# Optimization experiments

Measured on AMD Instinct MI355X. Metric: run time of the kernel, lower is better.

## Reference

```python
import jax, jax.numpy as jnp
import numpy as np

B, S, H = 4, 2048, 1024

def setup_inputs() -> dict:
    key = jax.random.key(0)
    ks = jax.random.split(key, 6)
    scale = 1.0 / np.sqrt(H)
    return {
        "query": jax.random.normal(ks[0], (B, S, H), dtype=jnp.float32),
        "key":   jax.random.normal(ks[1], (B, S, H), dtype=jnp.float32),
        "value": jax.random.normal(ks[2], (B, S, H), dtype=jnp.float32),
        "Wq": jax.random.normal(ks[3], (H, H), dtype=jnp.float32) * scale,
        "Wk": jax.random.normal(ks[4], (H, H), dtype=jnp.float32) * scale,
        "Wv": jax.random.normal(ks[5], (H, H), dtype=jnp.float32) * scale,
    }

def reference(query, key, value, Wq, Wk, Wv):
    # nn.Linear(bias=False): y = x @ W.T
    q = jnp.einsum('bsh,oh->bso', query, Wq)
    k = jnp.einsum('bsh,oh->bso', key, Wk)
    v = jnp.einsum('bsh,oh->bso', value, Wv)
    # full QK^T scores [B, Q, K], scaled by sqrt(hidden_size)
    scores = jnp.einsum('bqh,bkh->bqk', q, k) / jnp.sqrt(jnp.asarray(H, q.dtype))
    attn = jax.nn.softmax(scores, axis=2)
    return jnp.einsum('bqk,bkh->bqh', attn, v)
```

## Files before the change

### kernel.cpp

```cpp
#include <hip/hip_runtime.h>
#include <hip/hip_bf16.h>
#include <stdint.h>

#define BATCH 4
#define SLEN  2048
#define HID   1024

typedef __attribute__((ext_vector_type(8))) short bfrag8;
typedef __attribute__((ext_vector_type(4))) float facc4;

__device__ __forceinline__ unsigned short f2b(float f) {
  union { float f; unsigned int i; } x; x.f = f;
  unsigned int r = x.i + 0x7FFFu + ((x.i >> 16) & 1u);
  return (unsigned short)(r >> 16);
}
__device__ __forceinline__ unsigned int pk2(float a, float b) {
  unsigned int ua = __float_as_uint(a) + 0x8000u;
  unsigned int ub = __float_as_uint(b) + 0x8000u;
  return (ua >> 16) | (ub & 0xFFFF0000u);
}

__device__ __forceinline__ void gl_lds16(const void* g, void* l) {
  __builtin_amdgcn_global_load_lds(
      (const __attribute__((address_space(1))) void*)g,
      (__attribute__((address_space(3))) void*)l, 16, 0, 0);
}

__global__ __launch_bounds__(256) void qkv_proj(
    const float* __restrict__ q, const float* __restrict__ k,
    const float* __restrict__ v, const float* __restrict__ wq,
    const float* __restrict__ wk, const float* __restrict__ wv,
    unsigned short* __restrict__ Qb, unsigned short* __restrict__ Kb,
    unsigned short* __restrict__ Vt, float* __restrict__ lsum) {
  const int pid = blockIdx.x;
  if (pid < 8) {
    float4 z = {0.f, 0.f, 0.f, 0.f};
    ((float4*)lsum)[pid * 256 + threadIdx.x] = z;
  }
  const int p2     = (pid & 7) * 192 + (pid >> 3);
  const int g      = p2 >> 9;
  const int within = p2 & 511;

  const float* A; const float* B; unsigned short* C;
  long bm, bn; int ldc_;
  if (g == 0)      { A = q;  B = wq; C = Qb; }
  else if (g == 1) { A = k;  B = wk; C = Kb; }
  else             { A = wv; B = v;  C = Vt; }
  if (g < 2) {
    const int gid = within >> 5, rem = within & 31;
    bm = (long)(gid * 4 + (rem & 3)) * 128;
    bn = (long)(rem >> 2) * 128;
    ldc_ = 1024;
  } else {
    const int gid = within >> 8, rem = within & 255;
    bm = (long)(gid * 4 + (rem & 3)) * 128;
    bn = (long)(rem >> 2) * 128;
    ldc_ = 8192;
  }

  __shared__ __align__(16) unsigned short As[128 * 64];
  __shared__ __align__(16) unsigned short Bs[128 * 64];

  const int tid  = threadIdx.x;
  const int lane = tid & 63;
  const int wave = tid >> 6;
  const int wr   = (wave >> 1) * 64;
  const int wc   = (wave & 1) * 64;
  const int ln   = lane & 15;
  const int lq   = lane >> 4;
  const int swz  = ln & 7;

  facc4 acc[4][4] = {};

  const float* ap[4]; const float* bp[4];
  unsigned short* asd[4]; unsigned short* bsd[4];
#pragma unroll
  for (int j = 0; j < 4; ++j) {
    const int c   = j * 256 + tid;
    const int row = c >> 3;
    const int src = ((c & 7) ^ (row & 7)) * 8;
    ap[j]  = A + (bm + row) * 1024 + src;
    bp[j]  = B + (bn + row) * 1024 + src;
    asd[j] = &As[c * 8];
    bsd[j] = &Bs[c * 8];
  }

  for (int k0 = 0; k0 < 1024; k0 += 64) {
#pragma unroll
    for (int j = 0; j < 4; ++j) {
      const float4* a4 = (const float4*)ap[j];
      const float4* b4 = (const float4*)bp[j];
      float4 xa0 = a4[0], xa1 = a4[1];
      float4 xb0 = b4[0], xb1 = b4[1];
      ap[j] += 64; bp[j] += 64;
      uint4 wa = { pk2(xa0.x, xa0.y), pk2(xa0.z, xa0.w),
                   pk2(xa1.x, xa1.y), pk2(xa1.z, xa1.w) };
      uint4 wb = { pk2(xb0.x, xb0.y), pk2(xb0.z, xb0.w),
                   pk2(xb1.x, xb1.y), pk2(xb1.z, xb1.w) };
      *(uint4*)asd[j] = wa;
      *(uint4*)bsd[j] = wb;
    }
    __syncthreads();

#pragma unroll
    for (int kk = 0; kk < 2; ++kk) {
      bfrag8 af[4], bfr[4];
#pragma unroll
      for (int i = 0; i < 4; ++i)
        af[i] = *(const bfrag8*)&As[(wr + i * 16 + ln) * 64 + ((kk * 4 + lq) ^ swz) * 8];
#pragma unroll
      for (int j = 0; j < 4; ++j)
        bfr[j] = *(const bfrag8*)&Bs[(wc + j * 16 + ln) * 64 + ((kk * 4 + lq) ^ swz) * 8];
#pragma unroll
      for (int i = 0; i < 4; ++i)
#pragma unroll
        for (int j = 0; j < 4; ++j)
          acc[i][j] = __builtin_amdgcn_mfma_f32_16x16x32_bf16(af[i], bfr[j], acc[i][j], 0, 0, 0);
    }
    __syncthreads();
  }

#pragma unroll
  for (int i = 0; i < 4; ++i)
#pragma unroll
    for (int j = 0; j < 4; ++j) {
      const long m = bm + wr + i * 16 + lq * 4;
      const long n = bn + wc + j * 16 + ln;
#pragma unroll
      for (int r = 0; r < 4; ++r)
        C[(m + r) * (long)ldc_ + n] = f2b(acc[i][j][r]);
    }
}

template <int MODE, typename OutT>
__global__ __launch_bounds__(256) void gemm_nt(
    const unsigned short* __restrict__ A, const unsigned short* __restrict__ B,
    OutT* __restrict__ C, int K, int lda, int ldb, int ldc,
    long aStrideZ, long bStrideZ, long cStrideZ, float alpha,
    float* __restrict__ lsum) {
  A += (long)blockIdx.z * aStrideZ;
  B += (long)blockIdx.z * bStrideZ;
  C += (long)blockIdx.z * cStrideZ;
  const long lz = (long)blockIdx.z * SLEN;

  const int nbm = gridDim.x, nbn = gridDim.y;
  const int nb  = nbm * nbn;
  const int pid = blockIdx.y * nbm + blockIdx.x;
  const int p2  = (pid & 7) * (nb >> 3) + (pid >> 3);
  const int GROUP = 4;
  const int gsize = GROUP * nbn;
  const int gid   = p2 / gsize;
  const int rem   = p2 - gid * gsize;
  const long bm = (long)(gid * GROUP + (rem & (GROUP - 1))) * 128;
  const long bn = (long)(rem >> 2) * 128;

  __shared__ __align__(16) unsigned short As[128 * 64];
  __shared__ __align__(16) unsigned short Bs[128 * 64];

  const int tid  = threadIdx.x;
  const int lane = tid & 63;
  const int wave = tid >> 6;
  const int wr   = (wave >> 1) * 64;
  const int wc   = (wave & 1) * 64;
  const int ln   = lane & 15;
  const int lq   = lane >> 4;
  const int swz  = ln & 7;

  facc4 acc[4][4] = {};

  const unsigned short* ap[4]; const unsigned short* bp[4];
  unsigned short* asd[4]; unsigned short* bsd[4];
#pragma unroll
  for (int j = 0; j < 4; ++j) {
    const int c   = j * 256 + tid;
    const int row = c >> 3;
    const int src = ((c & 7) ^ (row & 7)) * 8;
    ap[j]  = A + (bm + row) * (long)lda + src;
    bp[j]  = B + (bn + row) * (long)ldb + src;
    asd[j] = &As[c * 8];
    bsd[j] = &Bs[c * 8];
  }

  for (int k0 = 0; k0 < K; k0 += 64) {
#pragma unroll
    for (int j = 0; j < 4; ++j) { gl_lds16(ap[j], asd[j]); ap[j] += 64; }
#pragma unroll
    for (int j = 0; j < 4; ++j) { gl_lds16(bp[j], bsd[j]); bp[j] += 64; }
    __syncthreads();

#pragma unroll
    for (int kk = 0; kk < 2; ++kk) {
      bfrag8 af[4], bfr[4];
#pragma unroll
      for (int i = 0; i < 4; ++i)
        af[i] = *(const bfrag8*)&As[(wr + i * 16 + ln) * 64 + ((kk * 4 + lq) ^ swz) * 8];
#pragma unroll
      for (int j = 0; j < 4; ++j)
        bfr[j] = *(const bfrag8*)&Bs[(wc + j * 16 + ln) * 64 + ((kk * 4 + lq) ^ swz) * 8];
#pragma unroll
      for (int i = 0; i < 4; ++i)
#pragma unroll
        for (int j = 0; j < 4; ++j)
          acc[i][j] = __builtin_amdgcn_mfma_f32_16x16x32_bf16(af[i], bfr[j], acc[i][j], 0, 0, 0);
    }
    __syncthreads();
  }

  if constexpr (MODE == 1) {
#pragma unroll
    for (int i = 0; i < 4; ++i) {
#pragma unroll
      for (int r = 0; r < 4; ++r) {
        const long m = bm + wr + i * 16 + lq * 4 + r;
        float rowsum = 0.f;
#pragma unroll
        for (int j = 0; j < 4; ++j) {
          const long n = bn + wc + j * 16 + ln;
          float e = __expf(acc[i][j][r] * alpha);
          C[m * (long)ldc + n] = (OutT)f2b(e);
          rowsum += e;
        }
        rowsum += __shfl_xor(rowsum, 1, 64);
        rowsum += __shfl_xor(rowsum, 2, 64);
        rowsum += __shfl_xor(rowsum, 4, 64);
        rowsum += __shfl_xor(rowsum, 8, 64);
        if (ln == 0) atomicAdd(&lsum[lz + m], rowsum);
      }
    }
  } else {
    float inv[16];
#pragma unroll
    for (int i = 0; i < 4; ++i)
#pragma unroll
      for (int r = 0; r < 4; ++r)
        inv[i * 4 + r] = 1.0f / lsum[lz + bm + wr + i * 16 + lq * 4 + r];
#pragma unroll
    for (int i = 0; i < 4; ++i)
#pragma unroll
      for (int j = 0; j < 4; ++j) {
        const long m = bm + wr + i * 16 + lq * 4;
        const long n = bn + wc + j * 16 + ln;
#pragma unroll
        for (int r = 0; r < 4; ++r)
          ((float*)C)[(m + r) * (long)ldc + n] = acc[i][j][r] * inv[i * 4 + r];
      }
  }
}

extern "C" void kernel_launch(void* const* d_in, const int* in_sizes, int n_in,
                              void* d_out, int out_size, void* d_ws, size_t ws_size,
                              hipStream_t stream) {
  const float* q_in = (const float*)d_in[0];
  const float* k_in = (const float*)d_in[1];
  const float* v_in = (const float*)d_in[2];
  const float* wq   = (const float*)d_in[3];
  const float* wk   = (const float*)d_in[4];
  const float* wv   = (const float*)d_in[5];
  float* out = (float*)d_out;

  const long NXH = (long)BATCH * SLEN * HID;
  const long SH  = (long)SLEN * HID;
  const long SS  = (long)SLEN * SLEN;

  unsigned short* ws  = (unsigned short*)d_ws;
  unsigned short* Qb  = ws;
  unsigned short* Kb  = Qb + NXH;
  unsigned short* Vt  = Kb + NXH;
  float*          lsum = (float*)(Vt + NXH);
  unsigned short* P   = (unsigned short*)(lsum + 8192);

  const dim3 blk(256);

  qkv_proj<<<dim3(1536), blk, 0, stream>>>(q_in, k_in, v_in, wq, wk, wv,
                                           Qb, Kb, Vt, lsum);

  gemm_nt<1, unsigned short><<<dim3(16, 16, BATCH), blk, 0, stream>>>(
      Qb, Kb, P, HID, HID, HID, SLEN, SH, SH, SS, 0.03125f, lsum);

  gemm_nt<2, float><<<dim3(16, 8, BATCH), blk, 0, stream>>>(
      P, Vt, out, SLEN, SLEN, BATCH * SLEN, HID, SS, SLEN, SH, 1.0f, lsum);
}
```

Before: 329.2 us.

## Pre-cast inputs and weights to bf16, then use direct global-to-LDS loads in projection

Adds a separate elementwise kernel that converts the fp32 activations and weights to bf16 in workspace. The projection GEMM then stages its tiles with global_load_lds DMA instead of loading fp32 into registers, converting and storing to LDS. This removes the redundant per-tile fp32 reads and conversions, since each input element was re-read by many tiles. The cost is an extra full read/write pass over roughly 27M floats and an extra launch. The P buffer now aliases the cast-input region, and rounding changes from round-half-up to round-to-nearest-even.

```diff
diff --git a/kernel.cpp b/kernel.cpp
--- a/kernel.cpp
+++ b/kernel.cpp
@@ -8,17 +8,13 @@
 
 typedef __attribute__((ext_vector_type(8))) short bfrag8;
 typedef __attribute__((ext_vector_type(4))) float facc4;
+typedef __attribute__((ext_vector_type(4))) unsigned short us4;
 
 __device__ __forceinline__ unsigned short f2b(float f) {
   union { float f; unsigned int i; } x; x.f = f;
   unsigned int r = x.i + 0x7FFFu + ((x.i >> 16) & 1u);
   return (unsigned short)(r >> 16);
 }
-__device__ __forceinline__ unsigned int pk2(float a, float b) {
-  unsigned int ua = __float_as_uint(a) + 0x8000u;
-  unsigned int ub = __float_as_uint(b) + 0x8000u;
-  return (ua >> 16) | (ub & 0xFFFF0000u);
-}
 
 __device__ __forceinline__ void gl_lds16(const void* g, void* l) {
   __builtin_amdgcn_global_load_lds(
@@ -26,26 +22,48 @@
       (__attribute__((address_space(3))) void*)l, 16, 0, 0);
 }
 
-__global__ __launch_bounds__(256) void qkv_proj(
+__global__ __launch_bounds__(256) void cast_all(
     const float* __restrict__ q, const float* __restrict__ k,
     const float* __restrict__ v, const float* __restrict__ wq,
     const float* __restrict__ wk, const float* __restrict__ wv,
+    us4* __restrict__ dst, float* __restrict__ lsum) {
+  if (blockIdx.x < 8) {
+    float4 z = {0.f, 0.f, 0.f, 0.f};
+    ((float4*)lsum)[blockIdx.x * 256 + threadIdx.x] = z;
+  }
+  const long i = (long)blockIdx.x * 256 + threadIdx.x;
+  const long S1 = 2097152, S2 = 4194304, S3 = 6291456,
+             S4 = 6553600, S5 = 6815744;
+  const float4* src; long off;
+  if (i < S2) {
+    if (i < S1) { src = (const float4*)q;  off = i; }
+    else        { src = (const float4*)k;  off = i - S1; }
+  } else if (i < S3) { src = (const float4*)v;  off = i - S2; }
+  else if   (i < S4) { src = (const float4*)wq; off = i - S3; }
+  else if   (i < S5) { src = (const float4*)wk; off = i - S4; }
+  else               { src = (const float4*)wv; off = i - S5; }
+  float4 x = src[off];
+  us4 o;
+  o.x = f2b(x.x); o.y = f2b(x.y); o.z = f2b(x.z); o.w = f2b(x.w);
+  dst[i] = o;
+}
+
+__global__ __launch_bounds__(256) void proj3(
+    const unsigned short* __restrict__ Xq, const unsigned short* __restrict__ Wqb,
+    const unsigned short* __restrict__ Xk, const unsigned short* __restrict__ Wkb,
+    const unsigned short* __restrict__ Xv, const unsigned short* __restrict__ Wvb,
     unsigned short* __restrict__ Qb, unsigned short* __restrict__ Kb,
-    unsigned short* __restrict__ Vt, float* __restrict__ lsum) {
+    unsigned short* __restrict__ Vt) {
   const int pid = blockIdx.x;
-  if (pid < 8) {
-    float4 z = {0.f, 0.f, 0.f, 0.f};
-    ((float4*)lsum)[pid * 256 + threadIdx.x] = z;
-  }
   const int p2     = (pid & 7) * 192 + (pid >> 3);
   const int g      = p2 >> 9;
   const int within = p2 & 511;
 
-  const float* A; const float* B; unsigned short* C;
+  const unsigned short* A; const unsigned short* B; unsigned short* C;
   long bm, bn; int ldc_;
-  if (g == 0)      { A = q;  B = wq; C = Qb; }
-  else if (g == 1) { A = k;  B = wk; C = Kb; }
-  else             { A = wv; B = v;  C = Vt; }
+  if (g == 0)      { A = Xq; B = Wqb; C = Qb; }
+  else if (g == 1) { A = Xk; B = Wkb; C = Kb; }
+  else             { A = Wvb; B = Xv; C = Vt; }
   if (g < 2) {
     const int gid = within >> 5, rem = within & 31;
     bm = (long)(gid * 4 + (rem & 3)) * 128;
@@ -72,7 +90,7 @@
 
   facc4 acc[4][4] = {};
 
-  const float* ap[4]; const float* bp[4];
+  const unsigned short* ap[4]; const unsigned short* bp[4];
   unsigned short* asd[4]; unsigned short* bsd[4];
 #pragma unroll
   for (int j = 0; j < 4; ++j) {
@@ -87,19 +105,9 @@
 
   for (int k0 = 0; k0 < 1024; k0 += 64) {
 #pragma unroll
-    for (int j = 0; j < 4; ++j) {
-      const float4* a4 = (const float4*)ap[j];
-      const float4* b4 = (const float4*)bp[j];
-      float4 xa0 = a4[0], xa1 = a4[1];
-      float4 xb0 = b4[0], xb1 = b4[1];
-      ap[j] += 64; bp[j] += 64;
-      uint4 wa = { pk2(xa0.x, xa0.y), pk2(xa0.z, xa0.w),
-                   pk2(xa1.x, xa1.y), pk2(xa1.z, xa1.w) };
-      uint4 wb = { pk2(xb0.x, xb0.y), pk2(xb0.z, xb0.w),
-                   pk2(xb1.x, xb1.y), pk2(xb1.z, xb1.w) };
-      *(uint4*)asd[j] = wa;
-      *(uint4*)bsd[j] = wb;
-    }
+    for (int j = 0; j < 4; ++j) { gl_lds16(ap[j], asd[j]); ap[j] += 64; }
+#pragma unroll
+    for (int j = 0; j < 4; ++j) { gl_lds16(bp[j], bsd[j]); bp[j] += 64; }
     __syncthreads();
 
 #pragma unroll
@@ -259,20 +267,29 @@
   float* out = (float*)d_out;
 
   const long NXH = (long)BATCH * SLEN * HID;
+  const long NW  = (long)HID * HID;
   const long SH  = (long)SLEN * HID;
   const long SS  = (long)SLEN * SLEN;
 
-  unsigned short* ws  = (unsigned short*)d_ws;
-  unsigned short* Qb  = ws;
-  unsigned short* Kb  = Qb + NXH;
-  unsigned short* Vt  = Kb + NXH;
+  unsigned short* ws = (unsigned short*)d_ws;
+  unsigned short* Xq  = ws;
+  unsigned short* Xk  = Xq  + NXH;
+  unsigned short* Xv  = Xk  + NXH;
+  unsigned short* Wqb = Xv  + NXH;
+  unsigned short* Wkb = Wqb + NW;
+  unsigned short* Wvb = Wkb + NW;
+  unsigned short* Qb  = Wvb + NW;
+  unsigned short* Kb  = Qb  + NXH;
+  unsigned short* Vt  = Kb  + NXH;
   float*          lsum = (float*)(Vt + NXH);
-  unsigned short* P   = (unsigned short*)(lsum + 8192);
+  unsigned short* P   = Xq;
 
   const dim3 blk(256);
 
-  qkv_proj<<<dim3(1536), blk, 0, stream>>>(q_in, k_in, v_in, wq, wk, wv,
-                                           Qb, Kb, Vt, lsum);
+  cast_all<<<dim3(27648), blk, 0, stream>>>(q_in, k_in, v_in, wq, wk, wv,
+                                            (us4*)ws, lsum);
+
+  proj3<<<dim3(1536), blk, 0, stream>>>(Xq, Wqb, Xk, Wkb, Xv, Wvb, Qb, Kb, Vt);
 
   gemm_nt<1, unsigned short><<<dim3(16, 16, BATCH), blk, 0, stream>>>(
       Qb, Kb, P, HID, HID, HID, SLEN, SH, SH, SS, 0.03125f, lsum);
```

Result: faster. 298.1 us (-9.5%).
